# Kernel tuning notes

Measured on AMD Instinct MI355X. Metric: run time of the kernel, lower is better.

Reference implementation:

```python
import jax, jax.numpy as jnp
import numpy as np

N_NODES = 20000
N_EDGES = 320000
NFEAT, NHID, NCLASS = 512, 256, 64


def setup_inputs() -> dict:
    key = jax.random.key(0)
    ks = jax.random.split(key, 8)
    x = jax.random.normal(ks[0], (N_NODES, NFEAT), dtype=jnp.float32)
    edge_index = jax.random.randint(ks[1], (2, N_EDGES), 0, N_NODES, dtype=jnp.int32)
    edge_weight = jax.random.uniform(ks[2], (N_EDGES,), dtype=jnp.float32)
    W1 = jax.random.normal(ks[3], (NFEAT, NHID), dtype=jnp.float32) / np.sqrt(NFEAT)
    b1 = jax.random.normal(ks[4], (NHID,), dtype=jnp.float32) * 0.01
    W2 = jax.random.normal(ks[5], (NHID, NCLASS), dtype=jnp.float32) / np.sqrt(NHID)
    b2 = jax.random.normal(ks[6], (NCLASS,), dtype=jnp.float32) * 0.01
    return {"x": x, "edge_index": edge_index, "edge_weight": edge_weight,
            "W1": W1, "b1": b1, "W2": W2, "b2": b2}


def reference(x, edge_index, edge_weight, W1, b1, W2, b2):
    # GraphConvolution: out = adj @ (x @ W) + b, adj given as weighted edge list
    row, col = edge_index[0], edge_index[1]
    n = x.shape[0]

    def gcn(h, W, b):
        support = h @ W                                   # [N, d_out]
        msgs = edge_weight[:, None] * support[col]        # gather: [E, d_out]
        agg = jax.ops.segment_sum(msgs, row, num_segments=n)  # scatter-add
        return agg + b

    h = jax.nn.selu(gcn(x, W1, b1))        # [N, nhid]
    h = jax.nn.selu(gcn(h, W2, b2))        # [N, nclass]
    pooled = jax.nn.selu(jnp.mean(h, axis=0, keepdims=True))  # [1, nclass]
    # dropout is identity at eval time
    return jax.nn.log_softmax(pooled, axis=1)
```

## Files before the change

kernel.cpp:

```cpp
#include <hip/hip_runtime.h>
#include <math.h>

#define N_NODES 20000
#define N_EDGES 320000
#define NFEAT 512
#define NHID 256
#define NCLASS 64

typedef __attribute__((ext_vector_type(8))) short bf16x8;
typedef __attribute__((ext_vector_type(4))) float f32x4;

__device__ __forceinline__ float selu_f(float x) {
    const float alpha = 1.6732632423543772f;
    const float scale = 1.0507009873554805f;
    return x > 0.f ? scale * x : scale * alpha * (expf(x) - 1.f);
}

__device__ __forceinline__ short f2bf(float f) {
    unsigned u = __builtin_bit_cast(unsigned, f);
    unsigned r = (u + 0x7FFFu + ((u >> 16) & 1u)) >> 16;
    return (short)r;
}

__device__ __forceinline__ float bf2f(unsigned short b) {
    unsigned u = ((unsigned)b) << 16;
    return __builtin_bit_cast(float, u);
}

#define EDGE_BLOCKS ((N_EDGES + 255) / 256)
#define W1_TILES ((NFEAT / 32) * (NHID / 32))
#define W2_TILES ((NHID / 32) * (NCLASS / 32))
__global__ __launch_bounds__(256) void k_count_cast(
    const int* __restrict__ row, int* __restrict__ counts,
    const float* __restrict__ W1, const float* __restrict__ W2,
    short* __restrict__ w1t, short* __restrict__ w2t)
{
    __shared__ float tile[32][33];
    int b = blockIdx.x, tid = threadIdx.x;
    if (b < EDGE_BLOCKS) {
        int e = b * 256 + tid;
        if (e < N_EDGES) atomicAdd(&counts[row[e]], 1);
        return;
    }
    int t = b - EDGE_BLOCKS;
    const float* W; short* Wt; int K, N, tk, tn;
    if (t < W1_TILES) { W = W1; Wt = w1t; K = NFEAT; N = NHID; tk = t & 15; tn = t >> 4; }
    else { t -= W1_TILES; W = W2; Wt = w2t; K = NHID; N = NCLASS; tk = t & 7; tn = t >> 3; }
    int c = tid & 31, r0 = tid >> 5;
    int k0 = tk * 32, n0 = tn * 32;
    #pragma unroll
    for (int i = 0; i < 4; ++i) {
        int r = r0 + i * 8;
        tile[r][c] = W[(size_t)(k0 + r) * N + n0 + c];
    }
    __syncthreads();
    #pragma unroll
    for (int i = 0; i < 4; ++i) {
        int r = r0 + i * 8;
        Wt[(size_t)(n0 + r) * K + k0 + c] = f2bf(tile[c][r]);
    }
}

__global__ __launch_bounds__(1024) void k_scan(const int* __restrict__ counts,
                                               int* __restrict__ row_ptr,
                                               int* __restrict__ write_ptr) {
    __shared__ int wsum[16];
    int tid = threadIdx.x, lane = tid & 63, wave = tid >> 6;
    int base = tid * 20;
    int v[20];
    int s = 0;
    #pragma unroll
    for (int j = 0; j < 20; ++j) {
        int i = base + j;
        int c = (i < N_NODES) ? counts[i] : 0;
        v[j] = s;
        s += c;
    }
    int ws = s;
    #pragma unroll
    for (int d = 1; d < 64; d <<= 1) {
        int t = __shfl_up(ws, d);
        if (lane >= d) ws += t;
    }
    if (lane == 63) wsum[wave] = ws;
    __syncthreads();
    if (wave == 0) {
        int t = (lane < 16) ? wsum[lane] : 0;
        #pragma unroll
        for (int d = 1; d < 16; d <<= 1) {
            int u = __shfl_up(t, d);
            if (lane >= d) t += u;
        }
        if (lane < 16) wsum[lane] = t;
    }
    __syncthreads();
    int off = (wave ? wsum[wave - 1] : 0) + (ws - s);
    #pragma unroll
    for (int j = 0; j < 20; ++j) {
        int i = base + j;
        if (i < N_NODES) { row_ptr[i] = off + v[j]; write_ptr[i] = off + v[j]; }
    }
    if (tid == 0) row_ptr[N_NODES] = wsum[15];
}

__global__ void k_scatter(const int* __restrict__ row, const int* __restrict__ col,
                          const float* __restrict__ w, int* __restrict__ write_ptr,
                          int2* __restrict__ epack) {
    int e = blockIdx.x * blockDim.x + threadIdx.x;
    if (e < N_EDGES) {
        int r = row[e];
        int pos = atomicAdd(&write_ptr[r], 1);
        epack[pos] = make_int2(col[e], __builtin_bit_cast(int, w[e]));
    }
}

template<int BM, int BN, int BK, int MREP, int NREP, bool AFP32>
__global__ __launch_bounds__(256) void k_gemm_bf16(
    const void* __restrict__ Av, const short* __restrict__ Bt,
    short* __restrict__ C, int M, int N, int K)
{
    constexpr int LDT = BK + 8;
    __shared__ short As[BM * LDT];
    __shared__ short Bs[BN * LDT];
    const int tid = threadIdx.x;
    const int lane = tid & 63;
    const int w = tid >> 6;
    const int wr = w >> 1, wc = w & 1;
    const int m0 = blockIdx.x * BM, n0 = blockIdx.y * BN;
    constexpr int SEGS = BK / 8;
    constexpr int A_ITER = BM * SEGS / 256;
    constexpr int B_ITER = BN * SEGS / 256;

    f32x4 acc[MREP][NREP] = {};

    for (int kt = 0; kt < K; kt += BK) {
        #pragma unroll
        for (int it = 0; it < A_ITER; ++it) {
            int idx = tid + it * 256;
            int r = idx / SEGS, seg = idx % SEGS;
            int gr = m0 + r; if (gr >= M) gr = M - 1;
            bf16x8 o;
            if constexpr (AFP32) {
                const float* ap = (const float*)Av + (size_t)gr * K + kt + seg * 8;
                float4 p0 = *(const float4*)ap, p1 = *(const float4*)(ap + 4);
                o[0] = f2bf(p0.x); o[1] = f2bf(p0.y); o[2] = f2bf(p0.z); o[3] = f2bf(p0.w);
                o[4] = f2bf(p1.x); o[5] = f2bf(p1.y); o[6] = f2bf(p1.z); o[7] = f2bf(p1.w);
            } else {
                o = *(const bf16x8*)((const short*)Av + (size_t)gr * K + kt + seg * 8);
            }
            *(bf16x8*)(As + r * LDT + seg * 8) = o;
        }
        #pragma unroll
        for (int it = 0; it < B_ITER; ++it) {
            int idx = tid + it * 256;
            int r = idx / SEGS, seg = idx % SEGS;
            *(bf16x8*)(Bs + r * LDT + seg * 8) =
                *(const bf16x8*)(Bt + (size_t)(n0 + r) * K + kt + seg * 8);
        }
        __syncthreads();
        #pragma unroll
        for (int ks = 0; ks < BK / 32; ++ks) {
            bf16x8 a[MREP], b[NREP];
            #pragma unroll
            for (int m = 0; m < MREP; ++m)
                a[m] = *(const bf16x8*)(As + (wr * (BM / 2) + m * 16 + (lane & 15)) * LDT
                                        + ks * 32 + (lane >> 4) * 8);
            #pragma unroll
            for (int n = 0; n < NREP; ++n)
                b[n] = *(const bf16x8*)(Bs + (wc * (BN / 2) + n * 16 + (lane & 15)) * LDT
                                        + ks * 32 + (lane >> 4) * 8);
            #pragma unroll
            for (int m = 0; m < MREP; ++m)
                #pragma unroll
                for (int n = 0; n < NREP; ++n)
                    acc[m][n] = __builtin_amdgcn_mfma_f32_16x16x32_bf16(a[m], b[n], acc[m][n], 0, 0, 0);
        }
        __syncthreads();
    }
    #pragma unroll
    for (int m = 0; m < MREP; ++m) {
        #pragma unroll
        for (int n = 0; n < NREP; ++n) {
            #pragma unroll
            for (int r = 0; r < 4; ++r) {
                int grow = m0 + wr * (BM / 2) + m * 16 + (lane >> 4) * 4 + r;
                int gcol = n0 + wc * (BN / 2) + n * 16 + (lane & 15);
                if (grow < M) C[(size_t)grow * N + gcol] = f2bf(acc[m][n][r]);
            }
        }
    }
}

__global__ __launch_bounds__(256) void k_agg1(const short* __restrict__ support,
                                              const int* __restrict__ row_ptr,
                                              const int2* __restrict__ epack,
                                              const float* __restrict__ b1,
                                              short* __restrict__ h1) {
    int wid = (blockIdx.x * 256 + threadIdx.x) >> 6;
    int lane = threadIdx.x & 63;
    if (wid >= N_NODES) return;
    int e0 = row_ptr[wid], e1 = row_ptr[wid + 1];
    float a0[4] = {}, a1[4] = {}, a2[4] = {}, a3[4] = {};
    int e = e0;
    for (; e + 4 <= e1; e += 4) {
        int2 m0 = epack[e + 0], m1 = epack[e + 1], m2 = epack[e + 2], m3 = epack[e + 3];
        ushort4 v0 = *(const ushort4*)(support + (size_t)m0.x * NHID + lane * 4);
        ushort4 v1 = *(const ushort4*)(support + (size_t)m1.x * NHID + lane * 4);
        ushort4 v2 = *(const ushort4*)(support + (size_t)m2.x * NHID + lane * 4);
        ushort4 v3 = *(const ushort4*)(support + (size_t)m3.x * NHID + lane * 4);
        float w0 = __builtin_bit_cast(float, m0.y), w1 = __builtin_bit_cast(float, m1.y);
        float w2 = __builtin_bit_cast(float, m2.y), w3 = __builtin_bit_cast(float, m3.y);
        a0[0] = fmaf(w0, bf2f(v0.x), a0[0]); a0[1] = fmaf(w0, bf2f(v0.y), a0[1]);
        a0[2] = fmaf(w0, bf2f(v0.z), a0[2]); a0[3] = fmaf(w0, bf2f(v0.w), a0[3]);
        a1[0] = fmaf(w1, bf2f(v1.x), a1[0]); a1[1] = fmaf(w1, bf2f(v1.y), a1[1]);
        a1[2] = fmaf(w1, bf2f(v1.z), a1[2]); a1[3] = fmaf(w1, bf2f(v1.w), a1[3]);
        a2[0] = fmaf(w2, bf2f(v2.x), a2[0]); a2[1] = fmaf(w2, bf2f(v2.y), a2[1]);
        a2[2] = fmaf(w2, bf2f(v2.z), a2[2]); a2[3] = fmaf(w2, bf2f(v2.w), a2[3]);
        a3[0] = fmaf(w3, bf2f(v3.x), a3[0]); a3[1] = fmaf(w3, bf2f(v3.y), a3[1]);
        a3[2] = fmaf(w3, bf2f(v3.z), a3[2]); a3[3] = fmaf(w3, bf2f(v3.w), a3[3]);
    }
    for (; e < e1; ++e) {
        int2 m = epack[e];
        float wgt = __builtin_bit_cast(float, m.y);
        ushort4 v = *(const ushort4*)(support + (size_t)m.x * NHID + lane * 4);
        a0[0] = fmaf(wgt, bf2f(v.x), a0[0]); a0[1] = fmaf(wgt, bf2f(v.y), a0[1]);
        a0[2] = fmaf(wgt, bf2f(v.z), a0[2]); a0[3] = fmaf(wgt, bf2f(v.w), a0[3]);
    }
    ushort4 o;
    o.x = (unsigned short)f2bf(selu_f(a0[0] + a1[0] + a2[0] + a3[0] + b1[lane * 4 + 0]));
    o.y = (unsigned short)f2bf(selu_f(a0[1] + a1[1] + a2[1] + a3[1] + b1[lane * 4 + 1]));
    o.z = (unsigned short)f2bf(selu_f(a0[2] + a1[2] + a2[2] + a3[2] + b1[lane * 4 + 2]));
    o.w = (unsigned short)f2bf(selu_f(a0[3] + a1[3] + a2[3] + a3[3] + b1[lane * 4 + 3]));
    *(ushort4*)(h1 + (size_t)wid * NHID + lane * 4) = o;
}

#define AGG2_BLOCKS (N_NODES / 8)
__global__ __launch_bounds__(256) void k_agg2(const short* __restrict__ support2,
                                              const int* __restrict__ row_ptr,
                                              const int2* __restrict__ epack,
                                              const float* __restrict__ b2,
                                              float* __restrict__ partial) {
    __shared__ float bsum[4][64];
    int tid = threadIdx.x, lane = tid & 63, wave = tid >> 6;
    float bias = b2[lane];
    float local = 0.f;
    #pragma unroll
    for (int q = 0; q < 2; ++q) {
        int node = blockIdx.x * 8 + wave * 2 + q;
        int e0 = row_ptr[node], e1 = row_ptr[node + 1];
        float s0 = 0.f, s1 = 0.f, s2 = 0.f, s3 = 0.f;
        int e = e0;
        for (; e + 4 <= e1; e += 4) {
            int2 m0 = epack[e + 0], m1 = epack[e + 1], m2 = epack[e + 2], m3 = epack[e + 3];
            float v0 = bf2f((unsigned short)support2[(size_t)m0.x * NCLASS + lane]);
            float v1 = bf2f((unsigned short)support2[(size_t)m1.x * NCLASS + lane]);
            float v2 = bf2f((unsigned short)support2[(size_t)m2.x * NCLASS + lane]);
            float v3 = bf2f((unsigned short)support2[(size_t)m3.x * NCLASS + lane]);
            s0 = fmaf(__builtin_bit_cast(float, m0.y), v0, s0);
            s1 = fmaf(__builtin_bit_cast(float, m1.y), v1, s1);
            s2 = fmaf(__builtin_bit_cast(float, m2.y), v2, s2);
            s3 = fmaf(__builtin_bit_cast(float, m3.y), v3, s3);
        }
        for (; e < e1; ++e) {
            int2 m = epack[e];
            s0 = fmaf(__builtin_bit_cast(float, m.y),
                      bf2f((unsigned short)support2[(size_t)m.x * NCLASS + lane]), s0);
        }
        local += selu_f(s0 + s1 + s2 + s3 + bias);
    }
    bsum[wave][lane] = local;
    __syncthreads();
    if (tid < 64)
        partial[(size_t)blockIdx.x * 64 + tid] =
            bsum[0][tid] + bsum[1][tid] + bsum[2][tid] + bsum[3][tid];
}

#define RED_BLOCKS 50
#define RED_ROWS (AGG2_BLOCKS / RED_BLOCKS)
__global__ __launch_bounds__(256) void k_reduce1(const float* __restrict__ partial,
                                                 float* __restrict__ stage2) {
    __shared__ float red[4][64];
    int tid = threadIdx.x, lane = tid & 63, sl = tid >> 6;
    int r0 = blockIdx.x * RED_ROWS;
    float s = 0.f;
    for (int i = sl; i < RED_ROWS; i += 4)
        s += partial[(size_t)(r0 + i) * 64 + lane];
    red[sl][lane] = s;
    __syncthreads();
    if (tid < 64)
        stage2[(size_t)blockIdx.x * 64 + tid] =
            red[0][tid] + red[1][tid] + red[2][tid] + red[3][tid];
}

__global__ void k_final(const float* __restrict__ stage2, float* __restrict__ out) {
    int lane = threadIdx.x;
    float tot = 0.f;
    #pragma unroll
    for (int i = 0; i < RED_BLOCKS; ++i)
        tot += stage2[(size_t)i * 64 + lane];
    float v = selu_f(tot * (1.0f / N_NODES));
    float m = v;
    #pragma unroll
    for (int off = 32; off >= 1; off >>= 1) m = fmaxf(m, __shfl_xor(m, off));
    float ex = expf(v - m);
    float ssum = ex;
    #pragma unroll
    for (int off = 32; off >= 1; off >>= 1) ssum += __shfl_xor(ssum, off);
    out[lane] = v - m - logf(ssum);
}

extern "C" void kernel_launch(void* const* d_in, const int* in_sizes, int n_in,
                              void* d_out, int out_size, void* d_ws, size_t ws_size,
                              hipStream_t stream) {
    const float* x  = (const float*)d_in[0];
    const int* ei   = (const int*)d_in[1];
    const float* ew = (const float*)d_in[2];
    const float* W1 = (const float*)d_in[3];
    const float* b1 = (const float*)d_in[4];
    const float* W2 = (const float*)d_in[5];
    const float* b2 = (const float*)d_in[6];
    float* out = (float*)d_out;
    const int* e_row = ei;
    const int* e_col = ei + N_EDGES;

    char* p = (char*)d_ws;
    short* w1t      = (short*)p;  p += (size_t)NHID * NFEAT * 2;
    short* w2t      = (short*)p;  p += (size_t)NCLASS * NHID * 2;
    short* support1 = (short*)p;  p += (size_t)N_NODES * NHID * 2;
    short* h1       = (short*)p;  p += (size_t)N_NODES * NHID * 2;
    int* counts     = (int*)p;    p += (size_t)N_NODES * 4;
    int* row_ptr    = (int*)p;    p += (size_t)(N_NODES + 1) * 4;
    int* write_ptr  = (int*)p;    p += (size_t)N_NODES * 4;
    int2* epack     = (int2*)p;   p += (size_t)N_EDGES * 8;
    float* partial  = (float*)p;  p += (size_t)AGG2_BLOCKS * 64 * 4;
    float* stage2   = (float*)p;  p += (size_t)RED_BLOCKS * 64 * 4;
    short* support2 = support1;

    hipMemsetAsync(counts, 0, (size_t)N_NODES * 4, stream);

    k_count_cast<<<EDGE_BLOCKS + W1_TILES + W2_TILES, 256, 0, stream>>>(
        e_row, counts, W1, W2, w1t, w2t);
    k_scan<<<1, 1024, 0, stream>>>(counts, row_ptr, write_ptr);
    k_scatter<<<(N_EDGES + 255) / 256, 256, 0, stream>>>(e_row, e_col, ew, write_ptr, epack);

    k_gemm_bf16<64, 256, 64, 2, 8, true>
        <<<dim3((N_NODES + 63) / 64, NHID / 256), 256, 0, stream>>>(
            x, w1t, support1, N_NODES, NHID, NFEAT);
    k_agg1<<<(N_NODES * 64 + 255) / 256, 256, 0, stream>>>(support1, row_ptr, epack, b1, h1);

    k_gemm_bf16<64, 64, 32, 2, 2, false>
        <<<dim3((N_NODES + 63) / 64, NCLASS / 64), 256, 0, stream>>>(
            h1, w2t, support2, N_NODES, NCLASS, NHID);
    k_agg2<<<AGG2_BLOCKS, 256, 0, stream>>>(support2, row_ptr, epack, b2, partial);
    k_reduce1<<<RED_BLOCKS, 256, 0, stream>>>(partial, stage2);
    k_final<<<1, 64, 0, stream>>>(stage2, out);
}
```

Before: 225.3 us.

## Fuse layer-1 aggregation with layer-2 GEMM through shared memory

The layer-1 gather/SELU kernel and the second bf16 GEMM become one kernel. Each 512-thread block aggregates 32 nodes into a padded LDS tile, then runs MFMA against W2 to write support2 directly. This removes the h1 round trip through global memory and one kernel launch. support2 now gets its own buffer instead of aliasing support1, and each block does four nodes per wave serially, which may lower latency hiding in the gather.

```diff
diff --git a/kernel.cpp b/kernel.cpp
--- a/kernel.cpp
+++ b/kernel.cpp
@@ -191,47 +191,72 @@
     }
 }
 
-__global__ __launch_bounds__(256) void k_agg1(const short* __restrict__ support,
-                                              const int* __restrict__ row_ptr,
-                                              const int2* __restrict__ epack,
-                                              const float* __restrict__ b1,
-                                              short* __restrict__ h1) {
-    int wid = (blockIdx.x * 256 + threadIdx.x) >> 6;
-    int lane = threadIdx.x & 63;
-    if (wid >= N_NODES) return;
-    int e0 = row_ptr[wid], e1 = row_ptr[wid + 1];
-    float a0[4] = {}, a1[4] = {}, a2[4] = {}, a3[4] = {};
-    int e = e0;
-    for (; e + 4 <= e1; e += 4) {
-        int2 m0 = epack[e + 0], m1 = epack[e + 1], m2 = epack[e + 2], m3 = epack[e + 3];
-        ushort4 v0 = *(const ushort4*)(support + (size_t)m0.x * NHID + lane * 4);
-        ushort4 v1 = *(const ushort4*)(support + (size_t)m1.x * NHID + lane * 4);
-        ushort4 v2 = *(const ushort4*)(support + (size_t)m2.x * NHID + lane * 4);
-        ushort4 v3 = *(const ushort4*)(support + (size_t)m3.x * NHID + lane * 4);
-        float w0 = __builtin_bit_cast(float, m0.y), w1 = __builtin_bit_cast(float, m1.y);
-        float w2 = __builtin_bit_cast(float, m2.y), w3 = __builtin_bit_cast(float, m3.y);
-        a0[0] = fmaf(w0, bf2f(v0.x), a0[0]); a0[1] = fmaf(w0, bf2f(v0.y), a0[1]);
-        a0[2] = fmaf(w0, bf2f(v0.z), a0[2]); a0[3] = fmaf(w0, bf2f(v0.w), a0[3]);
-        a1[0] = fmaf(w1, bf2f(v1.x), a1[0]); a1[1] = fmaf(w1, bf2f(v1.y), a1[1]);
-        a1[2] = fmaf(w1, bf2f(v1.z), a1[2]); a1[3] = fmaf(w1, bf2f(v1.w), a1[3]);
-        a2[0] = fmaf(w2, bf2f(v2.x), a2[0]); a2[1] = fmaf(w2, bf2f(v2.y), a2[1]);
-        a2[2] = fmaf(w2, bf2f(v2.z), a2[2]); a2[3] = fmaf(w2, bf2f(v2.w), a2[3]);
-        a3[0] = fmaf(w3, bf2f(v3.x), a3[0]); a3[1] = fmaf(w3, bf2f(v3.y), a3[1]);
-        a3[2] = fmaf(w3, bf2f(v3.z), a3[2]); a3[3] = fmaf(w3, bf2f(v3.w), a3[3]);
-    }
-    for (; e < e1; ++e) {
-        int2 m = epack[e];
-        float wgt = __builtin_bit_cast(float, m.y);
-        ushort4 v = *(const ushort4*)(support + (size_t)m.x * NHID + lane * 4);
-        a0[0] = fmaf(wgt, bf2f(v.x), a0[0]); a0[1] = fmaf(wgt, bf2f(v.y), a0[1]);
-        a0[2] = fmaf(wgt, bf2f(v.z), a0[2]); a0[3] = fmaf(wgt, bf2f(v.w), a0[3]);
-    }
-    ushort4 o;
-    o.x = (unsigned short)f2bf(selu_f(a0[0] + a1[0] + a2[0] + a3[0] + b1[lane * 4 + 0]));
-    o.y = (unsigned short)f2bf(selu_f(a0[1] + a1[1] + a2[1] + a3[1] + b1[lane * 4 + 1]));
-    o.z = (unsigned short)f2bf(selu_f(a0[2] + a1[2] + a2[2] + a3[2] + b1[lane * 4 + 2]));
-    o.w = (unsigned short)f2bf(selu_f(a0[3] + a1[3] + a2[3] + a3[3] + b1[lane * 4 + 3]));
-    *(ushort4*)(h1 + (size_t)wid * NHID + lane * 4) = o;
+#define H1LD 264
+__global__ __launch_bounds__(512) void k_agg1_gemm2(
+    const short* __restrict__ support, const int* __restrict__ row_ptr,
+    const int2* __restrict__ epack, const float* __restrict__ b1,
+    const short* __restrict__ w2t, short* __restrict__ support2)
+{
+    __shared__ short h1s[32 * H1LD];
+    int tid = threadIdx.x, lane = tid & 63, w = tid >> 6;
+    int nbase = blockIdx.x * 32;
+
+    #pragma unroll
+    for (int q = 0; q < 4; ++q) {
+        int nl = w * 4 + q;
+        int node = nbase + nl;
+        int e0 = row_ptr[node], e1 = row_ptr[node + 1];
+        float a0[4] = {}, a1[4] = {}, a2[4] = {}, a3[4] = {};
+        int e = e0;
+        for (; e + 4 <= e1; e += 4) {
+            int2 m0 = epack[e + 0], m1 = epack[e + 1], m2 = epack[e + 2], m3 = epack[e + 3];
+            ushort4 v0 = *(const ushort4*)(support + (size_t)m0.x * NHID + lane * 4);
+            ushort4 v1 = *(const ushort4*)(support + (size_t)m1.x * NHID + lane * 4);
+            ushort4 v2 = *(const ushort4*)(support + (size_t)m2.x * NHID + lane * 4);
+            ushort4 v3 = *(const ushort4*)(support + (size_t)m3.x * NHID + lane * 4);
+            float w0 = __builtin_bit_cast(float, m0.y), w1 = __builtin_bit_cast(float, m1.y);
+            float w2 = __builtin_bit_cast(float, m2.y), w3 = __builtin_bit_cast(float, m3.y);
+            a0[0] = fmaf(w0, bf2f(v0.x), a0[0]); a0[1] = fmaf(w0, bf2f(v0.y), a0[1]);
+            a0[2] = fmaf(w0, bf2f(v0.z), a0[2]); a0[3] = fmaf(w0, bf2f(v0.w), a0[3]);
+            a1[0] = fmaf(w1, bf2f(v1.x), a1[0]); a1[1] = fmaf(w1, bf2f(v1.y), a1[1]);
+            a1[2] = fmaf(w1, bf2f(v1.z), a1[2]); a1[3] = fmaf(w1, bf2f(v1.w), a1[3]);
+            a2[0] = fmaf(w2, bf2f(v2.x), a2[0]); a2[1] = fmaf(w2, bf2f(v2.y), a2[1]);
+            a2[2] = fmaf(w2, bf2f(v2.z), a2[2]); a2[3] = fmaf(w2, bf2f(v2.w), a2[3]);
+            a3[0] = fmaf(w3, bf2f(v3.x), a3[0]); a3[1] = fmaf(w3, bf2f(v3.y), a3[1]);
+            a3[2] = fmaf(w3, bf2f(v3.z), a3[2]); a3[3] = fmaf(w3, bf2f(v3.w), a3[3]);
+        }
+        for (; e < e1; ++e) {
+            int2 m = epack[e];
+            float wgt = __builtin_bit_cast(float, m.y);
+            ushort4 v = *(const ushort4*)(support + (size_t)m.x * NHID + lane * 4);
+            a0[0] = fmaf(wgt, bf2f(v.x), a0[0]); a0[1] = fmaf(wgt, bf2f(v.y), a0[1]);
+            a0[2] = fmaf(wgt, bf2f(v.z), a0[2]); a0[3] = fmaf(wgt, bf2f(v.w), a0[3]);
+        }
+        ushort4 o;
+        o.x = (unsigned short)f2bf(selu_f(a0[0] + a1[0] + a2[0] + a3[0] + b1[lane * 4 + 0]));
+        o.y = (unsigned short)f2bf(selu_f(a0[1] + a1[1] + a2[1] + a3[1] + b1[lane * 4 + 1]));
+        o.z = (unsigned short)f2bf(selu_f(a0[2] + a1[2] + a2[2] + a3[2] + b1[lane * 4 + 2]));
+        o.w = (unsigned short)f2bf(selu_f(a0[3] + a1[3] + a2[3] + a3[3] + b1[lane * 4 + 3]));
+        *(ushort4*)(h1s + nl * H1LD + lane * 4) = o;
+    }
+    __syncthreads();
+
+    int tr = w >> 2, tc = w & 3;
+    f32x4 acc = {};
+    #pragma unroll
+    for (int kk = 0; kk < NHID / 32; ++kk) {
+        bf16x8 a = *(const bf16x8*)(h1s + (tr * 16 + (lane & 15)) * H1LD
+                                    + kk * 32 + (lane >> 4) * 8);
+        bf16x8 b = *(const bf16x8*)(w2t + (size_t)(tc * 16 + (lane & 15)) * NHID
+                                    + kk * 32 + (lane >> 4) * 8);
+        acc = __builtin_amdgcn_mfma_f32_16x16x32_bf16(a, b, acc, 0, 0, 0);
+    }
+    #pragma unroll
+    for (int r = 0; r < 4; ++r) {
+        int grow = nbase + tr * 16 + (lane >> 4) * 4 + r;
+        int gcol = tc * 16 + (lane & 15);
+        support2[(size_t)grow * NCLASS + gcol] = f2bf(acc[r]);
+    }
 }
 
 #define AGG2_BLOCKS (N_NODES / 8)
@@ -327,14 +352,13 @@
     short* w1t      = (short*)p;  p += (size_t)NHID * NFEAT * 2;
     short* w2t      = (short*)p;  p += (size_t)NCLASS * NHID * 2;
     short* support1 = (short*)p;  p += (size_t)N_NODES * NHID * 2;
-    short* h1       = (short*)p;  p += (size_t)N_NODES * NHID * 2;
     int* counts     = (int*)p;    p += (size_t)N_NODES * 4;
     int* row_ptr    = (int*)p;    p += (size_t)(N_NODES + 1) * 4;
     int* write_ptr  = (int*)p;    p += (size_t)N_NODES * 4;
     int2* epack     = (int2*)p;   p += (size_t)N_EDGES * 8;
     float* partial  = (float*)p;  p += (size_t)AGG2_BLOCKS * 64 * 4;
     float* stage2   = (float*)p;  p += (size_t)RED_BLOCKS * 64 * 4;
-    short* support2 = support1;
+    short* support2 = (short*)p;  p += (size_t)N_NODES * NCLASS * 2;
 
     hipMemsetAsync(counts, 0, (size_t)N_NODES * 4, stream);
 
@@ -346,11 +370,10 @@
     k_gemm_bf16<64, 256, 64, 2, 8, true>
         <<<dim3((N_NODES + 63) / 64, NHID / 256), 256, 0, stream>>>(
             x, w1t, support1, N_NODES, NHID, NFEAT);
-    k_agg1<<<(N_NODES * 64 + 255) / 256, 256, 0, stream>>>(support1, row_ptr, epack, b1, h1);
-
-    k_gemm_bf16<64, 64, 32, 2, 2, false>
-        <<<dim3((N_NODES + 63) / 64, NCLASS / 64), 256, 0, stream>>>(
-            h1, w2t, support2, N_NODES, NCLASS, NHID);
+
+    k_agg1_gemm2<<<N_NODES / 32, 512, 0, stream>>>(
+        support1, row_ptr, epack, b1, w2t, support2);
+
     k_agg2<<<AGG2_BLOCKS, 256, 0, stream>>>(support2, row_ptr, epack, b2, partial);
     k_reduce1<<<RED_BLOCKS, 256, 0, stream>>>(partial, stage2);
     k_final<<<1, 64, 0, stream>>>(stage2, out);
```

Result: faster. 217.7 us (-3.4%).
